# Kernel optimization log

Hardware: AMD Instinct MI355X
Metric: run time of the kernel (lower is better)

## Reference

```python
import jax, jax.numpy as jnp
import numpy as np

B, L, IN_DIM, D, H, NCONV = 64, 400, 500, 128, 8, 4
HD = D // H  # head dim = 16


def _conv1d(x, w, b, pad, groups=1):
    # x: [B, L, Cin], w: [k, Cin//groups, Cout]
    y = jax.lax.conv_general_dilated(
        x, w, window_strides=(1,), padding=[(pad, pad)],
        dimension_numbers=('NWC', 'WIO', 'NWC'), feature_group_count=groups)
    return y + b


def _layernorm(x, g, b, eps=1e-5):
    mu = jnp.mean(x, axis=-1, keepdims=True)
    var = jnp.mean(jnp.square(x - mu), axis=-1, keepdims=True)
    return (x - mu) * jax.lax.rsqrt(var + eps) * g + b


def _posenc(L, d):
    pos = jnp.arange(L, dtype=jnp.float32)[:, None]                 # [L,1]
    div = jnp.exp(jnp.arange(0, d, 2, dtype=jnp.float32) * (-jnp.log(10000.0) / d))
    ang = pos * div                                                 # [L, d/2]
    return jnp.stack([jnp.sin(ang), jnp.cos(ang)], axis=-1).reshape(L, d)


def setup_inputs() -> dict:
    key = jax.random.key(0)
    ks = jax.random.split(key, 24)
    s = lambda k, shape, scale: jax.random.normal(k, shape, dtype=jnp.float32) * scale
    inp = {
        'x': s(ks[0], (B, L, IN_DIM), 1.0),
        # init conv: k=5, 500 -> 128
        'w_init': s(ks[1], (5, IN_DIM, D), 0.02),
        'b_init': jnp.zeros((D,), jnp.float32),
        # 4 depthwise-separable conv layers (pre-LN, residual): depthwise k=7
        'ln_conv_g': jnp.ones((NCONV, D), jnp.float32),
        'ln_conv_b': jnp.zeros((NCONV, D), jnp.float32),
        'w_dw': s(ks[2], (NCONV, 7, 1, D), 0.1),
        'b_dw': jnp.zeros((NCONV, D), jnp.float32),
        'w_pw': s(ks[3], (NCONV, 1, D, D), 0.05),
        'b_pw': jnp.zeros((NCONV, D), jnp.float32),
        # self-attention (pre-LN, residual)
        'ln_att_g': jnp.ones((D,), jnp.float32),
        'ln_att_b': jnp.zeros((D,), jnp.float32),
        'wq': s(ks[4], (D, D), 0.05), 'bq': jnp.zeros((D,), jnp.float32),
        'wk': s(ks[5], (D, D), 0.05), 'bk': jnp.zeros((D,), jnp.float32),
        'wv': s(ks[6], (D, D), 0.05), 'bv': jnp.zeros((D,), jnp.float32),
        'wo': s(ks[7], (D, D), 0.05), 'bo': jnp.zeros((D,), jnp.float32),
        # FFN (pre-LN, residual)
        'ln_ffn_g': jnp.ones((D,), jnp.float32),
        'ln_ffn_b': jnp.zeros((D,), jnp.float32),
        'w1': s(ks[8], (D, D), 0.05), 'b1': jnp.zeros((D,), jnp.float32),
        'w2': s(ks[9], (D, D), 0.05), 'b2': jnp.zeros((D,), jnp.float32),
    }
    return inp


def reference(x, w_init, b_init, ln_conv_g, ln_conv_b, w_dw, b_dw, w_pw, b_pw,
              ln_att_g, ln_att_b, wq, bq, wk, bk, wv, bv, wo, bo,
              ln_ffn_g, ln_ffn_b, w1, b1, w2, b2):
    # 1) init conv (Conv1d k=5 pad=2, 500 -> 128); torch permutes, equivalent NWC conv
    h = _conv1d(x, w_init, b_init, pad=2)                    # [B, L, D]
    # 2) positional encoding
    h = h + _posenc(h.shape[1], D)
    for i in range(NCONV):
        res = h
        h = _layernorm(h, ln_conv_g[i], ln_conv_b[i])
        h = _conv1d(h, w_dw[i], b_dw[i], pad=3, groups=D)    # depthwise k=7
        h = _conv1d(h, w_pw[i], b_pw[i], pad=0)              # pointwise 1x1
        h = jax.nn.relu(h) + res
    # 4) multi-head self-attention, pre-LN + residual
    res = h
    hn = _layernorm(h, ln_att_g, ln_att_b)
    q = (hn @ wq + bq).reshape(B, L, H, HD)
    k = (hn @ wk + bk).reshape(B, L, H, HD)
    v = (hn @ wv + bv).reshape(B, L, H, HD)
    scores = jnp.einsum('bqhd,bkhd->bhqk', q, k) / jnp.sqrt(jnp.float32(HD))
    attn = jax.nn.softmax(scores, axis=-1)
    o = jnp.einsum('bhqk,bkhd->bqhd', attn, v).reshape(B, L, D)
    h = o @ wo + bo + res
    # 5) FFN, pre-LN + residual
    res = h
    hn = _layernorm(h, ln_ffn_g, ln_ffn_b)
    h = jax.nn.relu(hn @ w1 + b1) @ w2 + b2 + res
    return h
```

## Files before the change

### kernel.cpp

```cpp
#include <hip/hip_runtime.h>
#include <hip/hip_bf16.h>
#include <math.h>

#define B 64
#define L 400
#define IN_DIM 500
#define D 128
#define H 8
#define HD 16
#define NCONV 4
#define BL (B*L)

typedef __attribute__((ext_vector_type(8))) unsigned short ushort8;
typedef __attribute__((ext_vector_type(8))) short bf16x8;
typedef __attribute__((ext_vector_type(4))) float f32x4;

__device__ __forceinline__ unsigned short f2bf(float f) {
    unsigned u = __float_as_uint(f);
    unsigned r = (u + 0x7fffu + ((u >> 16) & 1u)) >> 16;
    return (unsigned short)r;
}
__device__ __forceinline__ float bf2f(unsigned short u) {
    return __uint_as_float(((unsigned)u) << 16);
}

__device__ __forceinline__ void gload16(const void* g, void* l) {
    __builtin_amdgcn_global_load_lds(
        (const __attribute__((address_space(1))) unsigned int*)g,
        (__attribute__((address_space(3))) unsigned int*)l,
        16, 0, 0);
}

__global__ __launch_bounds__(256) void k_cvt_x(
        const float* __restrict__ x, unsigned short* __restrict__ xb) {
    int idx = blockIdx.x * 256 + threadIdx.x;
    int row = idx >> 6, ch = idx & 63;
    int b = row / 404, rr = row - b * 404;
    ushort8 o = (ushort8)0;
    if (rr >= 2 && rr < 402) {
        int l = rr - 2;
        const float* src = x + ((size_t)b * 400 + l) * 500 + ch * 8;
        if (ch < 62) {
            float4 v0 = *(const float4*)(src);
            float4 v1 = *(const float4*)(src + 4);
            o[0] = f2bf(v0.x); o[1] = f2bf(v0.y); o[2] = f2bf(v0.z); o[3] = f2bf(v0.w);
            o[4] = f2bf(v1.x); o[5] = f2bf(v1.y); o[6] = f2bf(v1.z); o[7] = f2bf(v1.w);
        } else {
#pragma unroll
            for (int j = 0; j < 8; ++j) {
                int c = ch * 8 + j;
                o[j] = (c < 500) ? f2bf(src[j]) : (unsigned short)0;
            }
        }
    }
    *(ushort8*)(xb + (size_t)idx * 8) = o;
}

__global__ __launch_bounds__(256) void k_cvt_w(
        const float* __restrict__ w, unsigned short* __restrict__ wbt) {
    int idx = blockIdx.x * 256 + threadIdx.x;
    int k = idx & 511, n = (idx >> 9) & 127, t = idx >> 16;
    float v = (k < 500) ? w[((size_t)t * 500 + k) * 128 + n] : 0.f;
    wbt[idx] = f2bf(v);
}

__global__ __launch_bounds__(256) void k_cvt_wall(
        const float* w0, const float* w1, const float* w2, const float* w3,
        const float* w4, const float* w5, const float* w6, const float* w7,
        const float* w8, const float* w9, unsigned short* __restrict__ out) {
    const float* arr[10] = {w0,w1,w2,w3,w4,w5,w6,w7,w8,w9};
    int widx = blockIdx.x >> 6;
    const float* w = arr[widx];
    int idx = ((blockIdx.x & 63) << 8) + threadIdx.x;
    int n = idx >> 7, k = idx & 127;
    out[(size_t)widx * 16384 + idx] = f2bf(w[k * 128 + n]);
}

#define TM 80
#define BK 64
__global__ __launch_bounds__(256) void k_initconv_mfma(
        const unsigned short* __restrict__ xb,
        const unsigned short* __restrict__ wbt,
        const float* __restrict__ bias, float* __restrict__ out) {
    __shared__ unsigned short As[84 * BK];
    __shared__ unsigned short Ws[5][64 * BK];
    int tid = threadIdx.x;
    int b = blockIdx.x / 10;
    int rem = blockIdx.x - b * 10;
    int l0 = (rem >> 1) * TM;
    int nh = rem & 1;
    int lane = tid & 63, wave = tid >> 6;
    int kgrp = lane >> 4, lm = lane & 15;

    f32x4 acc[5];
#pragma unroll
    for (int mf = 0; mf < 5; ++mf) acc[mf] = (f32x4)0.f;

    const unsigned short* abase = xb + ((size_t)(b * 404 + l0)) * 512;
    const unsigned short* wbase = wbt + (size_t)nh * 64 * 512;

    for (int k0 = 0; k0 < 512; k0 += BK) {
        for (int idx = tid; idx < 672; idx += 256) {
            int r = idx >> 3, sc = idx & 7;
            gload16(abase + (size_t)r * 512 + k0 + ((sc ^ (r & 7)) * 8),
                    As + idx * 8);
        }
#pragma unroll
        for (int i = 0; i < 10; ++i) {
            int idx = tid + i * 256;
            int t = idx >> 9;
            int sub = idx & 511;
            int n = sub >> 3, sc = sub & 7;
            gload16(wbase + (size_t)t * 128 * 512 + (size_t)n * 512 + k0
                        + ((sc ^ (n & 7)) * 8),
                    &Ws[t][0] + sub * 8);
        }
        __syncthreads();
        int n16 = wave * 16 + lm;
#pragma unroll
        for (int ks = 0; ks < 2; ++ks) {
            int gc = ks * 4 + kgrp;
            bf16x8 bfr[5];
#pragma unroll
            for (int t = 0; t < 5; ++t)
                bfr[t] = *(const bf16x8*)(&Ws[t][0] + n16 * 64
                                          + ((gc ^ (n16 & 7)) * 8));
#pragma unroll
            for (int mf = 0; mf < 5; ++mf) {
#pragma unroll
                for (int t = 0; t < 5; ++t) {
                    int r = mf * 16 + lm + t;
                    bf16x8 af = *(const bf16x8*)(As + r * 64
                                                 + ((gc ^ (r & 7)) * 8));
                    acc[mf] = __builtin_amdgcn_mfma_f32_16x16x32_bf16(
                        af, bfr[t], acc[mf], 0, 0, 0);
                }
            }
        }
        __syncthreads();
    }

    {
        int n = nh * 64 + wave * 16 + lm;
        float bs = bias[n];
        float pbase = expf(-(float)(n & ~1) * (9.210340371976184f / 128.0f));
#pragma unroll
        for (int mf = 0; mf < 5; ++mf) {
#pragma unroll
            for (int r = 0; r < 4; ++r) {
                int l = l0 + mf * 16 + kgrp * 4 + r;
                float ang = (float)l * pbase;
                float pe = (n & 1) ? cosf(ang) : sinf(ang);
                out[((size_t)b * 400 + l) * 128 + n] = acc[mf][r] + bs + pe;
            }
        }
    }
}

#define CB_ROWS 38
__global__ __launch_bounds__(256) void k_convblock(
        const float* __restrict__ hin, float* __restrict__ hout,
        const float* __restrict__ lng, const float* __restrict__ lnb,
        const float* __restrict__ wdw, const float* __restrict__ bdw,
        const unsigned short* __restrict__ wpt, const float* __restrict__ bpw) {
    __shared__ unsigned short Ws[128 * 128];
    __shared__ unsigned short Ln[CB_ROWS * 128];
    __shared__ unsigned short Dw[32 * 128];
    int tid = threadIdx.x;
    int b = blockIdx.x / 13;
    int tile = blockIdx.x - b * 13;
    int l0 = tile * 32;
    int lv = (l0 + 32 <= L) ? 32 : (L - l0);
    int lane = tid & 63, wave = tid >> 6;
    int lm = lane & 15, kgrp = lane >> 4;

#pragma unroll
    for (int i = 0; i < 8; ++i) {
        int idx = tid + i * 256;
        int n = idx >> 4, sc = idx & 15;
        gload16(wpt + (size_t)n * 128 + ((sc ^ (n & 15)) * 8), Ws + idx * 8);
    }

    {
        float2 gg = *(const float2*)(lng + lane * 2);
        float2 bb = *(const float2*)(lnb + lane * 2);
#pragma unroll
        for (int ri = 0; ri < 10; ++ri) {
            int r = wave + ri * 4;
            if (r < CB_ROWS) {
                int gl = l0 - 3 + r;
                bool ok = (gl >= 0 && gl < L);
                float2 v = make_float2(0.f, 0.f);
                if (ok) v = *(const float2*)(hin + ((size_t)b * L + gl) * 128 + lane * 2);
                float s = v.x + v.y, q = v.x * v.x + v.y * v.y;
#pragma unroll
                for (int off = 32; off; off >>= 1) {
                    s += __shfl_xor(s, off);
                    q += __shfl_xor(q, off);
                }
                float mu  = s * (1.f / 128.f);
                float var = q * (1.f / 128.f) - mu * mu;
                float inv = rsqrtf(var + 1e-5f);
                unsigned pk = 0;
                if (ok) {
                    float ox = (v.x - mu) * inv * gg.x + bb.x;
                    float oy = (v.y - mu) * inv * gg.y + bb.y;
                    pk = (unsigned)f2bf(ox) | ((unsigned)f2bf(oy) << 16);
                }
                *(unsigned*)(Ln + r * 128 + lane * 2) = pk;
            }
        }
    }
    __syncthreads();

    {
        int d = tid & 127, half = tid >> 7;
        float wr[7];
#pragma unroll
        for (int t = 0; t < 7; ++t) wr[t] = wdw[t * 128 + d];
        float bs = bdw[d];
        float win[7];
#pragma unroll
        for (int t = 0; t < 6; ++t) win[t] = bf2f(Ln[(half * 16 + t) * 128 + d]);
#pragma unroll
        for (int lj = 0; lj < 16; ++lj) {
            int l = half * 16 + lj;
            win[6] = bf2f(Ln[(l + 6) * 128 + d]);
            float a = bs;
#pragma unroll
            for (int t = 0; t < 7; ++t) a = fmaf(win[t], wr[t], a);
#pragma unroll
            for (int t = 0; t < 6; ++t) win[t] = win[t + 1];
            Dw[l * 128 + ((d >> 3) ^ (l & 15)) * 8 + (d & 7)] = f2bf(a);
        }
    }
    __syncthreads();

    f32x4 acc[2][2];
#pragma unroll
    for (int mf = 0; mf < 2; ++mf)
#pragma unroll
        for (int nt = 0; nt < 2; ++nt) acc[mf][nt] = (f32x4)0.f;
#pragma unroll
    for (int kc = 0; kc < 4; ++kc) {
        int c = kc * 4 + kgrp;
        bf16x8 af[2];
#pragma unroll
        for (int mf = 0; mf < 2; ++mf) {
            int r = mf * 16 + lm;
            af[mf] = *(const bf16x8*)(Dw + r * 128 + (c ^ (r & 15)) * 8);
        }
#pragma unroll
        for (int nt = 0; nt < 2; ++nt) {
            int n = wave * 32 + nt * 16 + lm;
            bf16x8 bfv = *(const bf16x8*)(Ws + n * 128 + (c ^ (n & 15)) * 8);
#pragma unroll
            for (int mf = 0; mf < 2; ++mf)
                acc[mf][nt] = __builtin_amdgcn_mfma_f32_16x16x32_bf16(
                    af[mf], bfv, acc[mf][nt], 0, 0, 0);
        }
    }

#pragma unroll
    for (int nt = 0; nt < 2; ++nt) {
        int n = wave * 32 + nt * 16 + lm;
        float bsn = bpw[n];
#pragma unroll
        for (int mf = 0; mf < 2; ++mf) {
#pragma unroll
            for (int r = 0; r < 4; ++r) {
                int row = mf * 16 + kgrp * 4 + r;
                if (row < lv) {
                    size_t gi = ((size_t)b * L + l0 + row) * 128 + n;
                    hout[gi] = fmaxf(acc[mf][nt][r] + bsn, 0.f) + hin[gi];
                }
            }
        }
    }
}

__global__ __launch_bounds__(256) void k_ln_gemm(
        const float* __restrict__ h, const float* __restrict__ g,
        const float* __restrict__ bta, const unsigned short* __restrict__ wt0,
        int nw, const float* __restrict__ bias0, const float* __restrict__ bias1,
        const float* __restrict__ bias2, unsigned short* __restrict__ out0,
        unsigned short* __restrict__ out1, unsigned short* __restrict__ out2,
        float s0, int relu) {
    __shared__ unsigned short As[32 * 128];
    __shared__ unsigned short Ws[128 * 128];
    int tid = threadIdx.x;
    int m0 = blockIdx.x * 32;
    int lane = tid & 63, wave = tid >> 6;
    int lm = lane & 15, kgrp = lane >> 4;
    int wm = wave >> 1, wn = wave & 1;

#pragma unroll
    for (int i = 0; i < 8; ++i) {
        int idx = tid + i * 256;
        int n = idx >> 4, sc = idx & 15;
        gload16(wt0 + (size_t)n * 128 + ((sc ^ (n & 15)) * 8), Ws + idx * 8);
    }

    {
        float2 gg = *(const float2*)(g + lane * 2);
        float2 bb = *(const float2*)(bta + lane * 2);
#pragma unroll
        for (int ri = 0; ri < 8; ++ri) {
            int r = wave + ri * 4;
            float2 v = *(const float2*)(h + ((size_t)m0 + r) * 128 + lane * 2);
            float s = v.x + v.y, q = v.x * v.x + v.y * v.y;
#pragma unroll
            for (int off = 32; off; off >>= 1) {
                s += __shfl_xor(s, off);
                q += __shfl_xor(q, off);
            }
            float mu  = s * (1.f / 128.f);
            float var = q * (1.f / 128.f) - mu * mu;
            float inv = rsqrtf(var + 1e-5f);
            float ox = (v.x - mu) * inv * gg.x + bb.x;
            float oy = (v.y - mu) * inv * gg.y + bb.y;
            unsigned pk = (unsigned)f2bf(ox) | ((unsigned)f2bf(oy) << 16);
            *(unsigned*)(As + r * 128 + ((lane >> 2) ^ (r & 15)) * 8
                         + ((lane * 2) & 7)) = pk;
        }
    }

    for (int i = 0; i < nw; ++i) {
        __syncthreads();
        f32x4 acc[4];
#pragma unroll
        for (int nt = 0; nt < 4; ++nt) acc[nt] = (f32x4)0.f;
#pragma unroll
        for (int kc = 0; kc < 4; ++kc) {
            int c = kc * 4 + kgrp;
            int r = wm * 16 + lm;
            bf16x8 af = *(const bf16x8*)(As + r * 128 + (c ^ (r & 15)) * 8);
#pragma unroll
            for (int nt = 0; nt < 4; ++nt) {
                int n = wn * 64 + nt * 16 + lm;
                bf16x8 bfv = *(const bf16x8*)(Ws + n * 128 + (c ^ (n & 15)) * 8);
                acc[nt] = __builtin_amdgcn_mfma_f32_16x16x32_bf16(
                    af, bfv, acc[nt], 0, 0, 0);
            }
        }
        const float* bias = (i == 0) ? bias0 : (i == 1) ? bias1 : bias2;
        unsigned short* out = (i == 0) ? out0 : (i == 1) ? out1 : out2;
        float sc0 = (i == 0) ? s0 : 1.f;
#pragma unroll
        for (int nt = 0; nt < 4; ++nt) {
            int n = wn * 64 + nt * 16 + lm;
            float bsn = bias[n];
#pragma unroll
            for (int r = 0; r < 4; ++r) {
                size_t m = (size_t)m0 + wm * 16 + kgrp * 4 + r;
                float v = acc[nt][r] + bsn;
                if (relu) v = fmaxf(v, 0.f);
                out[m * 128 + n] = f2bf(v * sc0);
            }
        }
        if (i + 1 < nw) {
            __syncthreads();
            const unsigned short* wp = wt0 + (size_t)(i + 1) * 16384;
#pragma unroll
            for (int j = 0; j < 8; ++j) {
                int idx = tid + j * 256;
                int n = idx >> 4, sc = idx & 15;
                gload16(wp + (size_t)n * 128 + ((sc ^ (n & 15)) * 8), Ws + idx * 8);
            }
        }
    }
}

__global__ __launch_bounds__(256) void k_gemm_bf16(
        const unsigned short* __restrict__ A,
        const unsigned short* __restrict__ Wt,
        const float* __restrict__ bias,
        const float* __restrict__ res,
        float* __restrict__ outf,
        unsigned short* __restrict__ outb,
        int relu, float oscale) {
    __shared__ unsigned short As[32 * 128];
    __shared__ unsigned short Ws[128 * 128];
    int tid = threadIdx.x;
    int m0 = blockIdx.x * 32;
    int lane = tid & 63, wave = tid >> 6;
    int lm = lane & 15, kgrp = lane >> 4;
    int wm = wave >> 1, wn = wave & 1;

#pragma unroll
    for (int i = 0; i < 2; ++i) {
        int idx = tid + i * 256;
        int r = idx >> 4, sc = idx & 15;
        gload16(A + ((size_t)(m0 + r)) * 128 + ((sc ^ (r & 15)) * 8), As + idx * 8);
    }
#pragma unroll
    for (int i = 0; i < 8; ++i) {
        int idx = tid + i * 256;
        int n = idx >> 4, sc = idx & 15;
        gload16(Wt + ((size_t)n) * 128 + ((sc ^ (n & 15)) * 8), Ws + idx * 8);
    }
    __syncthreads();

    f32x4 acc[4];
#pragma unroll
    for (int nt = 0; nt < 4; ++nt) acc[nt] = (f32x4)0.f;

#pragma unroll
    for (int kc = 0; kc < 4; ++kc) {
        int c = kc * 4 + kgrp;
        int r = wm * 16 + lm;
        bf16x8 af = *(const bf16x8*)(As + (r * 16 + (c ^ (r & 15))) * 8);
#pragma unroll
        for (int nt = 0; nt < 4; ++nt) {
            int n = wn * 64 + nt * 16 + lm;
            bf16x8 bfv = *(const bf16x8*)(Ws + (n * 16 + (c ^ (n & 15))) * 8);
            acc[nt] = __builtin_amdgcn_mfma_f32_16x16x32_bf16(af, bfv, acc[nt], 0, 0, 0);
        }
    }

#pragma unroll
    for (int nt = 0; nt < 4; ++nt) {
        int n = wn * 64 + nt * 16 + lm;
        float bs = bias[n];
#pragma unroll
        for (int r = 0; r < 4; ++r) {
            size_t m = (size_t)m0 + wm * 16 + kgrp * 4 + r;
            float v = acc[nt][r] + bs;
            if (relu) v = fmaxf(v, 0.f);
            if (res)  v += res[m * 128 + n];
            if (outf) outf[m * 128 + n] = v;
            else      outb[m * 128 + n] = f2bf(v * oscale);
        }
    }
}

#define KS 40
#define VS 424
__global__ __launch_bounds__(256) void k_attn_mfma(
        const unsigned short* __restrict__ qb,
        const unsigned short* __restrict__ kb,
        const unsigned short* __restrict__ vb,
        unsigned short* __restrict__ out) {
    __shared__ __align__(16) unsigned short Kpad[400 * KS];
    __shared__ __align__(16) unsigned short Vt[16 * VS];
    __shared__ __align__(16) unsigned short Ptmp[4][16 * KS];
    int tid = threadIdx.x;
    int b = blockIdx.x >> 3, h = blockIdx.x & 7;
    int lane = tid & 63, wave = tid >> 6;
    int lm = lane & 15, kgrp = lane >> 4;

    for (int idx = tid; idx < 800; idx += 256) {
        int l = idx >> 1, half = idx & 1;
        ushort8 kv = *(const ushort8*)(kb + ((size_t)(b * 400 + l)) * 128 + h * 16 + half * 8);
        *(ushort8*)(Kpad + l * KS + half * 8) = kv;
        *(ushort8*)(Kpad + l * KS + 16 + half * 8) = (ushort8)0;
    }
    for (int idx = tid; idx < 800; idx += 256) {
        int kk = idx >> 1, dh = idx & 1;
        ushort8 vv = *(const ushort8*)(vb + ((size_t)(b * 400 + kk)) * 128 + h * 16 + dh * 8);
#pragma unroll
        for (int j = 0; j < 8; ++j) Vt[(dh * 8 + j) * VS + kk] = vv[j];
    }
    {
        int d = tid >> 4, kk = 400 + (tid & 15);
        Vt[d * VS + kk] = 0;
    }
    __syncthreads();

    unsigned short* Pw = Ptmp[wave];
    for (int tt = wave; tt < 25; tt += 4) {
        int q0 = tt * 16;
        bf16x8 Qf = *(const bf16x8*)(qb + ((size_t)(b * 400 + q0 + lm)) * 128 + h * 16 + kgrp * 8);
        f32x4 s[25];
#pragma unroll
        for (int kt = 0; kt < 25; ++kt) {
            bf16x8 Kf = *(const bf16x8*)(Kpad + (kt * 16 + lm) * KS + kgrp * 8);
            s[kt] = __builtin_amdgcn_mfma_f32_16x16x32_bf16(Qf, Kf, (f32x4)0.f, 0, 0, 0);
        }
        float rmax[4], rsum[4];
#pragma unroll
        for (int r = 0; r < 4; ++r) rmax[r] = -1e30f;
#pragma unroll
        for (int kt = 0; kt < 25; ++kt)
#pragma unroll
            for (int r = 0; r < 4; ++r) rmax[r] = fmaxf(rmax[r], s[kt][r]);
#pragma unroll
        for (int mask = 1; mask <= 8; mask <<= 1)
#pragma unroll
            for (int r = 0; r < 4; ++r) rmax[r] = fmaxf(rmax[r], __shfl_xor(rmax[r], mask));
#pragma unroll
        for (int r = 0; r < 4; ++r) rsum[r] = 0.f;
#pragma unroll
        for (int kt = 0; kt < 25; ++kt)
#pragma unroll
            for (int r = 0; r < 4; ++r) {
                float p = __expf(s[kt][r] - rmax[r]);
                s[kt][r] = p;
                rsum[r] += p;
            }
#pragma unroll
        for (int mask = 1; mask <= 8; mask <<= 1)
#pragma unroll
            for (int r = 0; r < 4; ++r) rsum[r] += __shfl_xor(rsum[r], mask);
        float rinv[4];
#pragma unroll
        for (int r = 0; r < 4; ++r) rinv[r] = 1.f / rsum[r];

        f32x4 O = (f32x4)0.f;
#pragma unroll
        for (int kc = 0; kc < 13; ++kc) {
#pragma unroll
            for (int t = 0; t < 2; ++t) {
                int kt = kc * 2 + t;
#pragma unroll
                for (int r = 0; r < 4; ++r) {
                    unsigned short pv = (kt < 25) ? f2bf(s[kt][r]) : (unsigned short)0;
                    Pw[(kgrp * 4 + r) * KS + t * 16 + lm] = pv;
                }
            }
            __builtin_amdgcn_wave_barrier();
            __builtin_amdgcn_s_waitcnt(0);
            __builtin_amdgcn_wave_barrier();
            bf16x8 Pf = *(const bf16x8*)(Pw + lm * KS + kgrp * 8);
            bf16x8 Vf = *(const bf16x8*)(Vt + lm * VS + kc * 32 + kgrp * 8);
            O = __builtin_amdgcn_mfma_f32_16x16x32_bf16(Pf, Vf, O, 0, 0, 0);
            __builtin_amdgcn_wave_barrier();
        }
#pragma unroll
        for (int r = 0; r < 4; ++r) {
            int q = q0 + kgrp * 4 + r;
            out[((size_t)(b * 400 + q)) * 128 + h * 16 + lm] = f2bf(O[r] * rinv[r]);
        }
    }
}

extern "C" void kernel_launch(void* const* d_in, const int* in_sizes, int n_in,
                              void* d_out, int out_size, void* d_ws, size_t ws_size,
                              hipStream_t stream) {
    (void)in_sizes; (void)n_in; (void)out_size; (void)ws_size;
    const float* x      = (const float*)d_in[0];
    const float* w_init = (const float*)d_in[1];
    const float* b_init = (const float*)d_in[2];
    const float* lncg   = (const float*)d_in[3];
    const float* lncb   = (const float*)d_in[4];
    const float* w_dw   = (const float*)d_in[5];
    const float* b_dw   = (const float*)d_in[6];
    const float* w_pw   = (const float*)d_in[7];
    const float* b_pw   = (const float*)d_in[8];
    const float* lnag   = (const float*)d_in[9];
    const float* lnab   = (const float*)d_in[10];
    const float* wq     = (const float*)d_in[11];
    const float* bq     = (const float*)d_in[12];
    const float* wk     = (const float*)d_in[13];
    const float* bk     = (const float*)d_in[14];
    const float* wv     = (const float*)d_in[15];
    const float* bv     = (const float*)d_in[16];
    const float* wo     = (const float*)d_in[17];
    const float* bo     = (const float*)d_in[18];
    const float* lnfg   = (const float*)d_in[19];
    const float* lnfb   = (const float*)d_in[20];
    const float* w1     = (const float*)d_in[21];
    const float* b1     = (const float*)d_in[22];
    const float* w2     = (const float*)d_in[23];
    const float* b2     = (const float*)d_in[24];

    float* ws = (float*)d_ws;
    const size_t NBL = (size_t)BL * D;
    float* h0 = ws;
    float* outp = (float*)d_out;

    unsigned short* hnb = (unsigned short*)(ws + NBL);
    unsigned short* t0b = hnb + NBL;
    unsigned short* qb  = t0b + NBL;
    unsigned short* kb  = qb + NBL;
    unsigned short* vb  = kb + NBL;
    unsigned short* wt  = vb + NBL;
    unsigned short* xb  = wt + 10 * 16384;
    unsigned short* wbt = xb + (size_t)64 * 404 * 512;
    float* h1 = (float*)(wbt + (size_t)5 * 128 * 512);

    k_cvt_x<<<6464, 256, 0, stream>>>(x, xb);
    k_cvt_w<<<1280, 256, 0, stream>>>(w_init, wbt);
    k_cvt_wall<<<640, 256, 0, stream>>>(
        w_pw, w_pw + 16384, w_pw + 2 * 16384, w_pw + 3 * 16384,
        wq, wk, wv, wo, w1, w2, wt);

    k_initconv_mfma<<<640, 256, 0, stream>>>(xb, wbt, b_init, h0);

    for (int i = 0; i < NCONV; ++i) {
        const float* hin = (i & 1) ? h1 : h0;
        float* hout      = (i & 1) ? h0 : h1;
        k_convblock<<<832, 256, 0, stream>>>(
            hin, hout, lncg + i * D, lncb + i * D,
            w_dw + (size_t)i * 7 * D, b_dw + i * D,
            wt + (size_t)i * 16384, b_pw + i * D);
    }

    k_ln_gemm<<<800, 256, 0, stream>>>(h0, lnag, lnab, wt + 4 * 16384, 3,
                                       bq, bk, bv, qb, kb, vb, 0.25f, 0);
    k_attn_mfma<<<512, 256, 0, stream>>>(qb, kb, vb, t0b);
    k_gemm_bf16<<<800, 256, 0, stream>>>(t0b, wt + 7 * 16384, bo, h0,
                                         h0, nullptr, 0, 1.f);

    k_ln_gemm<<<800, 256, 0, stream>>>(h0, lnfg, lnfb, wt + 8 * 16384, 1,
                                       b1, nullptr, nullptr,
                                       t0b, nullptr, nullptr, 1.f, 1);
    k_gemm_bf16<<<800, 256, 0, stream>>>(t0b, wt + 9 * 16384, b2, h0,
                                         outp, nullptr, 0, 1.f);
}
```

Baseline: 341.0 us.

## Merge conversion kernels and widen attention blocks to eight waves

```diff
diff --git a/kernel.cpp b/kernel.cpp
--- a/kernel.cpp
+++ b/kernel.cpp
@@ -31,49 +31,51 @@
         16, 0, 0);
 }
 
-__global__ __launch_bounds__(256) void k_cvt_x(
-        const float* __restrict__ x, unsigned short* __restrict__ xb) {
-    int idx = blockIdx.x * 256 + threadIdx.x;
-    int row = idx >> 6, ch = idx & 63;
-    int b = row / 404, rr = row - b * 404;
-    ushort8 o = (ushort8)0;
-    if (rr >= 2 && rr < 402) {
-        int l = rr - 2;
-        const float* src = x + ((size_t)b * 400 + l) * 500 + ch * 8;
-        if (ch < 62) {
-            float4 v0 = *(const float4*)(src);
-            float4 v1 = *(const float4*)(src + 4);
-            o[0] = f2bf(v0.x); o[1] = f2bf(v0.y); o[2] = f2bf(v0.z); o[3] = f2bf(v0.w);
-            o[4] = f2bf(v1.x); o[5] = f2bf(v1.y); o[6] = f2bf(v1.z); o[7] = f2bf(v1.w);
-        } else {
-#pragma unroll
-            for (int j = 0; j < 8; ++j) {
-                int c = ch * 8 + j;
-                o[j] = (c < 500) ? f2bf(src[j]) : (unsigned short)0;
-            }
-        }
-    }
-    *(ushort8*)(xb + (size_t)idx * 8) = o;
-}
-
-__global__ __launch_bounds__(256) void k_cvt_w(
-        const float* __restrict__ w, unsigned short* __restrict__ wbt) {
-    int idx = blockIdx.x * 256 + threadIdx.x;
-    int k = idx & 511, n = (idx >> 9) & 127, t = idx >> 16;
-    float v = (k < 500) ? w[((size_t)t * 500 + k) * 128 + n] : 0.f;
-    wbt[idx] = f2bf(v);
-}
-
-__global__ __launch_bounds__(256) void k_cvt_wall(
-        const float* w0, const float* w1, const float* w2, const float* w3,
-        const float* w4, const float* w5, const float* w6, const float* w7,
-        const float* w8, const float* w9, unsigned short* __restrict__ out) {
-    const float* arr[10] = {w0,w1,w2,w3,w4,w5,w6,w7,w8,w9};
-    int widx = blockIdx.x >> 6;
-    const float* w = arr[widx];
-    int idx = ((blockIdx.x & 63) << 8) + threadIdx.x;
-    int n = idx >> 7, k = idx & 127;
-    out[(size_t)widx * 16384 + idx] = f2bf(w[k * 128 + n]);
+__global__ __launch_bounds__(256) void k_cvt_all(
+        const float* __restrict__ x, unsigned short* __restrict__ xb,
+        const float* __restrict__ w_init, unsigned short* __restrict__ wbt,
+        const float* __restrict__ w_pw, const float* __restrict__ wq,
+        const float* __restrict__ wk, const float* __restrict__ wv,
+        const float* __restrict__ wo, const float* __restrict__ w1,
+        const float* __restrict__ w2, unsigned short* __restrict__ wt) {
+    int bid = blockIdx.x;
+    if (bid < 6464) {
+        int idx = bid * 256 + threadIdx.x;
+        int row = idx >> 6, ch = idx & 63;
+        int b = row / 404, rr = row - b * 404;
+        ushort8 o = (ushort8)0;
+        if (rr >= 2 && rr < 402) {
+            int l = rr - 2;
+            const float* src = x + ((size_t)b * 400 + l) * 500 + ch * 8;
+            if (ch < 62) {
+                float4 v0 = *(const float4*)(src);
+                float4 v1 = *(const float4*)(src + 4);
+                o[0] = f2bf(v0.x); o[1] = f2bf(v0.y); o[2] = f2bf(v0.z); o[3] = f2bf(v0.w);
+                o[4] = f2bf(v1.x); o[5] = f2bf(v1.y); o[6] = f2bf(v1.z); o[7] = f2bf(v1.w);
+            } else {
+#pragma unroll
+                for (int j = 0; j < 8; ++j) {
+                    int c = ch * 8 + j;
+                    o[j] = (c < 500) ? f2bf(src[j]) : (unsigned short)0;
+                }
+            }
+        }
+        *(ushort8*)(xb + (size_t)idx * 8) = o;
+    } else if (bid < 7744) {
+        int idx = (bid - 6464) * 256 + threadIdx.x;
+        int k = idx & 511, n = (idx >> 9) & 127, t = idx >> 16;
+        float v = (k < 500) ? w_init[((size_t)t * 500 + k) * 128 + n] : 0.f;
+        wbt[idx] = f2bf(v);
+    } else {
+        int rb = bid - 7744;
+        const float* arr[10] = {w_pw, w_pw + 16384, w_pw + 2 * 16384,
+                                w_pw + 3 * 16384, wq, wk, wv, wo, w1, w2};
+        int widx = rb >> 6;
+        const float* w = arr[widx];
+        int idx = ((rb & 63) << 8) + threadIdx.x;
+        int n = idx >> 7, k = idx & 127;
+        wt[(size_t)widx * 16384 + idx] = f2bf(w[k * 128 + n]);
+    }
 }
 
 #define TM 80
@@ -192,7 +194,8 @@
                 bool ok = (gl >= 0 && gl < L);
                 float2 v = make_float2(0.f, 0.f);
                 if (ok) v = *(const float2*)(hin + ((size_t)b * L + gl) * 128 + lane * 2);
-                float s = v.x + v.y, q = v.x * v.x + v.y * v.y;
+                float s = v.x + v.y;
+                float q = v.x * v.x + v.y * v.y;
 #pragma unroll
                 for (int off = 32; off; off >>= 1) {
                     s += __shfl_xor(s, off);
@@ -308,7 +311,8 @@
         for (int ri = 0; ri < 8; ++ri) {
             int r = wave + ri * 4;
             float2 v = *(const float2*)(h + ((size_t)m0 + r) * 128 + lane * 2);
-            float s = v.x + v.y, q = v.x * v.x + v.y * v.y;
+            float s = v.x + v.y;
+            float q = v.x * v.x + v.y * v.y;
 #pragma unroll
             for (int off = 32; off; off >>= 1) {
                 s += __shfl_xor(s, off);
@@ -436,47 +440,49 @@
 
 #define KS 40
 #define VS 424
-__global__ __launch_bounds__(256) void k_attn_mfma(
+__global__ __launch_bounds__(512) void k_attn_mfma(
         const unsigned short* __restrict__ qb,
         const unsigned short* __restrict__ kb,
         const unsigned short* __restrict__ vb,
         unsigned short* __restrict__ out) {
     __shared__ __align__(16) unsigned short Kpad[400 * KS];
     __shared__ __align__(16) unsigned short Vt[16 * VS];
-    __shared__ __align__(16) unsigned short Ptmp[4][16 * KS];
+    __shared__ __align__(16) unsigned short Ptmp[8][16 * KS];
     int tid = threadIdx.x;
     int b = blockIdx.x >> 3, h = blockIdx.x & 7;
     int lane = tid & 63, wave = tid >> 6;
     int lm = lane & 15, kgrp = lane >> 4;
 
-    for (int idx = tid; idx < 800; idx += 256) {
+    for (int idx = tid; idx < 800; idx += 512) {
         int l = idx >> 1, half = idx & 1;
         ushort8 kv = *(const ushort8*)(kb + ((size_t)(b * 400 + l)) * 128 + h * 16 + half * 8);
         *(ushort8*)(Kpad + l * KS + half * 8) = kv;
         *(ushort8*)(Kpad + l * KS + 16 + half * 8) = (ushort8)0;
     }
-    for (int idx = tid; idx < 800; idx += 256) {
+    for (int idx = tid; idx < 800; idx += 512) {
         int kk = idx >> 1, dh = idx & 1;
         ushort8 vv = *(const ushort8*)(vb + ((size_t)(b * 400 + kk)) * 128 + h * 16 + dh * 8);
 #pragma unroll
         for (int j = 0; j < 8; ++j) Vt[(dh * 8 + j) * VS + kk] = vv[j];
     }
-    {
+    if (tid < 256) {
         int d = tid >> 4, kk = 400 + (tid & 15);
         Vt[d * VS + kk] = 0;
     }
     __syncthreads();
 
     unsigned short* Pw = Ptmp[wave];
-    for (int tt = wave; tt < 25; tt += 4) {
+    for (int tt = wave; tt < 25; tt += 8) {
         int q0 = tt * 16;
         bf16x8 Qf = *(const bf16x8*)(qb + ((size_t)(b * 400 + q0 + lm)) * 128 + h * 16 + kgrp * 8);
         f32x4 s[25];
+        __builtin_amdgcn_s_setprio(1);
 #pragma unroll
         for (int kt = 0; kt < 25; ++kt) {
             bf16x8 Kf = *(const bf16x8*)(Kpad + (kt * 16 + lm) * KS + kgrp * 8);
             s[kt] = __builtin_amdgcn_mfma_f32_16x16x32_bf16(Qf, Kf, (f32x4)0.f, 0, 0, 0);
         }
+        __builtin_amdgcn_s_setprio(0);
         float rmax[4], rsum[4];
 #pragma unroll
         for (int r = 0; r < 4; ++r) rmax[r] = -1e30f;
@@ -519,8 +525,8 @@
                 }
             }
             __builtin_amdgcn_wave_barrier();
-            __builtin_amdgcn_s_waitcnt(0);
-            __builtin_amdgcn_wave_barrier();
+            asm volatile("s_waitcnt lgkmcnt(0)" ::: "memory");
+            __builtin_amdgcn_sched_barrier(0);
             bf16x8 Pf = *(const bf16x8*)(Pw + lm * KS + kgrp * 8);
             bf16x8 Vf = *(const bf16x8*)(Vt + lm * VS + kc * 32 + kgrp * 8);
             O = __builtin_amdgcn_mfma_f32_16x16x32_bf16(Pf, Vf, O, 0, 0, 0);
@@ -579,11 +585,8 @@
     unsigned short* wbt = xb + (size_t)64 * 404 * 512;
     float* h1 = (float*)(wbt + (size_t)5 * 128 * 512);
 
-    k_cvt_x<<<6464, 256, 0, stream>>>(x, xb);
-    k_cvt_w<<<1280, 256, 0, stream>>>(w_init, wbt);
-    k_cvt_wall<<<640, 256, 0, stream>>>(
-        w_pw, w_pw + 16384, w_pw + 2 * 16384, w_pw + 3 * 16384,
-        wq, wk, wv, wo, w1, w2, wt);
+    k_cvt_all<<<8384, 256, 0, stream>>>(x, xb, w_init, wbt,
+                                        w_pw, wq, wk, wv, wo, w1, w2, wt);
 
     k_initconv_mfma<<<640, 256, 0, stream>>>(xb, wbt, b_init, h0);
 
@@ -598,7 +601,7 @@
 
     k_ln_gemm<<<800, 256, 0, stream>>>(h0, lnag, lnab, wt + 4 * 16384, 3,
                                        bq, bk, bv, qb, kb, vb, 0.25f, 0);
-    k_attn_mfma<<<512, 256, 0, stream>>>(qb, kb, vb, t0b);
+    k_attn_mfma<<<512, 512, 0, stream>>>(qb, kb, vb, t0b);
     k_gemm_bf16<<<800, 256, 0, stream>>>(t0b, wt + 7 * 16384, bo, h0,
                                          h0, nullptr, 0, 1.f);
 
```

After: 332.1 us. 1.03x faster.
